# Kernel optimization log

Measured on AMD Instinct MI355X. Metric: run time of the kernel, lower is better.

## Reference

```python
import jax, jax.numpy as jnp
import numpy as np

NEG_INF = -jnp.inf


def setup_inputs() -> dict:
    B, T, E, H = 16, 1024, 1024, 1024  # batch, seq, embed_dim, head_dim (T <= H required by original buffer slicing)
    key = jax.random.key(0)
    k1, k2, k3, k4, k5, k6 = jax.random.split(key, 6)
    return {
        "key": jax.random.normal(k1, (B, T, E), dtype=jnp.float32),
        "query": jax.random.normal(k2, (B, T, E), dtype=jnp.float32),
        "value": jax.random.normal(k3, (B, T, E), dtype=jnp.float32),
        "padding_mask": jnp.zeros((B, 1, T), dtype=jnp.int32),
        # nn.Linear(embed_dim, head_dim, bias=False) weights: [head_dim, embed_dim]
        "Wk": jax.random.normal(k4, (H, E), dtype=jnp.float32) * (E ** -0.5),
        "Wq": jax.random.normal(k5, (H, E), dtype=jnp.float32) * (E ** -0.5),
        "Wv": jax.random.normal(k6, (H, E), dtype=jnp.float32) * (E ** -0.5),
    }


def reference(key, query, value, padding_mask, Wk, Wq, Wv):
    # key/query/value: [B, T, E]; W*: [H, E]
    B, T, E = key.shape
    k = jnp.einsum("bte,he->bth", key, Wk)
    q = jnp.einsum("bte,he->bth", query, Wq)
    v = jnp.einsum("bte,he->bth", value, Wv)
    # NOTE: original scales by d_k = key.size(-1) = embed_dim, not head_dim
    scale = 1.0 / jnp.sqrt(jnp.float32(E))
    qk = jnp.einsum("bth,bsh->bts", q, k) * scale  # [B, T, T]
    # causal buffer is tril(ones, diagonal=1): position i can attend to j <= i+1
    causal = jnp.tril(jnp.ones((T, T), dtype=jnp.float32), k=1)
    qk = jnp.where(causal == 0, NEG_INF, qk)
    qk = jnp.where(padding_mask == 1, NEG_INF, qk)  # padding_mask broadcasts [B,1,T] -> [B,T,T]
    p = jax.nn.softmax(qk, axis=-1)
    attn = jnp.einsum("bts,bsh->bth", p, v)  # dropout is identity in eval mode
    return attn
```

## Files before the change

kernel.cpp:

```cpp
#include <hip/hip_runtime.h>
#include <hip/hip_bf16.h>
#include <stdint.h>

typedef __bf16 bf16;
typedef __attribute__((ext_vector_type(8))) __bf16 bf16x8;
typedef __attribute__((ext_vector_type(4))) __bf16 bf16x4;
typedef __attribute__((ext_vector_type(4))) float  f32x4;

static __device__ __forceinline__ void gll16(const void* g, void* lds_base) {
  __builtin_amdgcn_global_load_lds((__attribute__((address_space(1))) void*)g,
                                   (__attribute__((address_space(3))) void*)lds_base,
                                   16, 0, 0);
}

#define MFMA_CLUSTER(MQ)                                                       \
  __builtin_amdgcn_s_barrier();                                                \
  asm volatile("s_waitcnt lgkmcnt(0)" ::: "memory");                           \
  __builtin_amdgcn_sched_barrier(0);                                           \
  __builtin_amdgcn_s_setprio(1);                                               \
  _Pragma("unroll") for (int i_ = 0; i_ < 4; ++i_)                             \
  _Pragma("unroll") for (int n_ = 0; n_ < 4; ++n_)                             \
  _Pragma("unroll") for (int kh_ = 0; kh_ < 2; ++kh_)                          \
    acc[(MQ) * 4 + i_][n_] = __builtin_amdgcn_mfma_f32_16x16x32_bf16(          \
        af[i_][kh_], bfr[n_][kh_], acc[(MQ) * 4 + i_][n_], 0, 0, 0);           \
  __builtin_amdgcn_s_setprio(0);

template <int VARIANT>
__global__ __launch_bounds__(512, 2) void gemm8(const bf16* __restrict__ A,
                                                const bf16* __restrict__ B,
                                                bf16* __restrict__ Cb,
                                                float* __restrict__ Cf,
                                                const int* __restrict__ pad) {
  extern __shared__ char smem[];
  char* ldsA = smem;
  char* ldsB = smem + 65536;

  const int tid = threadIdx.x;
  const int lane = tid & 63, wave = tid >> 6;
  const int lo = lane & 15, hi = lane >> 4;
  const int wmi = wave >> 2, wni = wave & 3;
  const int swz = (lo & 7) << 4;

  const int nwg = gridDim.x;
  const int id = (blockIdx.x % 8) * (nwg >> 3) + blockIdx.x / 8;

  int row0, col0, nt, b = 0;
  if (VARIANT <= 1) {
    row0 = (id >> 2) * 256; col0 = (id & 3) * 256; nt = 16;
  } else {
    b = id >> 4;
    const int r = id & 15, it = r >> 2, jt = r & 3;
    row0 = it * 256; col0 = jt * 256;
    nt = (VARIANT == 3) ? min(16, 6 + 4 * it) : 16;
    if (VARIANT == 2 && jt > it) {
      bf16* Sb = Cb + ((size_t)b << 20);
      const bf16 NI = (bf16)(-__builtin_inff());
      bf16x8 fill = { NI, NI, NI, NI, NI, NI, NI, NI };
#pragma unroll
      for (int q = 0; q < 16; ++q) {
        const int off = (q * 512 + tid) * 8;
        const int rr = off >> 8, cc = off & 255;
        *(bf16x8*)(Sb + (size_t)(row0 + rr) * 1024 + col0 + cc) = fill;
      }
      return;
    }
  }
  const bf16* Ap = A + ((size_t)b << 20) + (size_t)row0 * 1024;
  const bf16* Bp = B + ((size_t)b << 20) + (size_t)col0 * 1024;
  const int ntm1 = nt - 1;

  auto stgA = [&](int tidx, int slot) {
    const int tc = tidx > ntm1 ? ntm1 : tidx;
#pragma unroll
    for (int r = 0; r < 4; ++r) {
      const int x  = (wave * 4 + r) * 1024 + lane * 16;
      const int xs = x ^ (((x >> 7) & 7) << 4);
      gll16((const char*)Ap + (size_t)(xs >> 7) * 2048 + (size_t)tc * 128 + (xs & 127),
            ldsA + slot * 32768 + (wave * 4 + r) * 1024);
    }
  };
  auto stgB = [&](int tidx, int slot) {
    const int tc = tidx > ntm1 ? ntm1 : tidx;
#pragma unroll
    for (int r = 0; r < 4; ++r) {
      const int x  = (wave * 4 + r) * 1024 + lane * 16;
      const int xs = x ^ (((x >> 7) & 7) << 4);
      gll16((const char*)Bp + (size_t)(xs >> 7) * 2048 + (size_t)tc * 128 + (xs & 127),
            ldsB + slot * 32768 + (wave * 4 + r) * 1024);
    }
  };

  f32x4 acc[8][4] = {};

  stgB(0, 0);
  stgA(0, 0);
  stgB(1, 1);
  asm volatile("s_waitcnt vmcnt(4)" ::: "memory");
  __builtin_amdgcn_s_barrier();

  bf16x8 af[4][2], bfr[4][2];
#pragma unroll 2
  for (int u = 0; u < nt; ++u) {
    const int cur = u & 1;
#pragma unroll
    for (int i_ = 0; i_ < 4; ++i_)
#pragma unroll
      for (int kh_ = 0; kh_ < 2; ++kh_) {
        const int row_ = wmi * 128 + i_ * 16 + lo;
        af[i_][kh_] = *(const bf16x8*)(ldsA + cur * 32768 +
                                       ((row_ * 128 + kh_ * 64 + hi * 16) ^ swz));
      }
#pragma unroll
    for (int n_ = 0; n_ < 4; ++n_)
#pragma unroll
      for (int kh_ = 0; kh_ < 2; ++kh_) {
        const int row_ = wni * 64 + n_ * 16 + lo;
        bfr[n_][kh_] = *(const bf16x8*)(ldsB + cur * 32768 +
                                        ((row_ * 128 + kh_ * 64 + hi * 16) ^ swz));
      }
    stgA(u + 1, cur ^ 1);
    MFMA_CLUSTER(0)
    __builtin_amdgcn_s_barrier();
#pragma unroll
    for (int i_ = 0; i_ < 4; ++i_)
#pragma unroll
      for (int kh_ = 0; kh_ < 2; ++kh_) {
        const int row_ = wmi * 128 + 64 + i_ * 16 + lo;
        af[i_][kh_] = *(const bf16x8*)(ldsA + cur * 32768 +
                                       ((row_ * 128 + kh_ * 64 + hi * 16) ^ swz));
      }
    stgB(u + 2, cur);
    MFMA_CLUSTER(1)
    asm volatile("s_waitcnt vmcnt(4)" ::: "memory");
    __builtin_amdgcn_s_barrier();
  }

  if (VARIANT == 0) {
#pragma unroll
    for (int m = 0; m < 8; ++m)
#pragma unroll
      for (int n = 0; n < 4; ++n) {
        const int c = col0 + wni * 64 + n * 16 + lo;
        const int rbase = row0 + wmi * 128 + m * 16 + hi * 4;
#pragma unroll
        for (int j = 0; j < 4; ++j)
          Cb[(size_t)(rbase + j) * 1024 + c] = (bf16)acc[m][n][j];
      }
  } else if (VARIANT == 1) {
#pragma unroll
    for (int m = 0; m < 8; ++m)
#pragma unroll
      for (int n = 0; n < 4; ++n) {
        const int r = row0 + wmi * 128 + m * 16 + hi * 4;
        const int c = col0 + wni * 64 + n * 16 + lo;
        const int bb = r >> 10, tt = r & 1023;
        bf16x4 h = { (bf16)acc[m][n][0], (bf16)acc[m][n][1],
                     (bf16)acc[m][n][2], (bf16)acc[m][n][3] };
        *(bf16x4*)(Cb + ((size_t)bb << 20) + ((size_t)c << 10) + tt) = h;
      }
  } else if (VARIANT == 2) {
    const float NINF = -__builtin_inff();
#pragma unroll
    for (int n = 0; n < 4; ++n) {
      const int s = col0 + wni * 64 + n * 16 + lo;
      const int pd = pad[(b << 10) + s];
#pragma unroll
      for (int m = 0; m < 8; ++m) {
        const int tbase = row0 + wmi * 128 + m * 16 + hi * 4;
#pragma unroll
        for (int j = 0; j < 4; ++j) {
          float v = acc[m][n][j] * 0.03125f;
          if (s > tbase + j + 1 || pd != 0) v = NINF;
          Cb[((size_t)b << 20) + (size_t)(tbase + j) * 1024 + s] = (bf16)v;
        }
      }
    }
  } else {
#pragma unroll
    for (int m = 0; m < 8; ++m)
#pragma unroll
      for (int n = 0; n < 4; ++n) {
        const int h2 = col0 + wni * 64 + n * 16 + lo;
        const int tbase = row0 + wmi * 128 + m * 16 + hi * 4;
#pragma unroll
        for (int j = 0; j < 4; ++j)
          Cf[((size_t)b << 20) + (size_t)(tbase + j) * 1024 + h2] = acc[m][n][j];
      }
  }
  asm volatile("s_waitcnt vmcnt(0)" ::: "memory");
}

__global__ __launch_bounds__(256) void cvt_kernel(const float* __restrict__ src,
                                                  bf16* __restrict__ dst, int n) {
  const int i = (blockIdx.x * 256 + threadIdx.x) * 8;
  if (i >= n) return;
  const f32x4 a = *(const f32x4*)(src + i);
  const f32x4 b = *(const f32x4*)(src + i + 4);
  bf16x8 o = { (bf16)a[0], (bf16)a[1], (bf16)a[2], (bf16)a[3],
               (bf16)b[0], (bf16)b[1], (bf16)b[2], (bf16)b[3] };
  *(bf16x8*)(dst + i) = o;
}

__global__ __launch_bounds__(64) void corner_kernel(const bf16* __restrict__ Q,
                                                    const bf16* __restrict__ K,
                                                    const int* __restrict__ pad,
                                                    bf16* __restrict__ S) {
  const int b = blockIdx.x / 3, it = blockIdx.x % 3;
  const int t = it * 256 + 255, s = (it + 1) * 256;
  const int lane = threadIdx.x;
  const bf16* q = Q + ((size_t)b << 20) + (size_t)t * 1024 + lane * 16;
  const bf16* k = K + ((size_t)b << 20) + (size_t)s * 1024 + lane * 16;
  bf16x8 q0 = *(const bf16x8*)q, q1 = *(const bf16x8*)(q + 8);
  bf16x8 k0 = *(const bf16x8*)k, k1 = *(const bf16x8*)(k + 8);
  float d = 0.f;
#pragma unroll
  for (int j = 0; j < 8; ++j) d += (float)q0[j] * (float)k0[j] + (float)q1[j] * (float)k1[j];
#pragma unroll
  for (int o = 32; o; o >>= 1) d += __shfl_xor(d, o, 64);
  if (lane == 0) {
    float v = d * 0.03125f;
    if (pad[(b << 10) + s] != 0) v = -__builtin_inff();
    S[((size_t)b << 20) + (size_t)t * 1024 + s] = (bf16)v;
  }
}

__global__ __launch_bounds__(256) void softmax_kernel(bf16* __restrict__ S) {
  const int row  = blockIdx.x * 4 + (threadIdx.x >> 6);
  const int lane = threadIdx.x & 63;
  bf16* r = S + (size_t)row * 1024 + lane * 16;
  bf16x8 v0 = *(const bf16x8*)r;
  bf16x8 v1 = *(const bf16x8*)(r + 8);
  float f[16];
#pragma unroll
  for (int j = 0; j < 8; ++j) { f[j] = (float)v0[j]; f[8 + j] = (float)v1[j]; }
  float m = f[0];
#pragma unroll
  for (int j = 1; j < 16; ++j) m = fmaxf(m, f[j]);
#pragma unroll
  for (int o = 32; o; o >>= 1) m = fmaxf(m, __shfl_xor(m, o, 64));
  float sum = 0.f;
#pragma unroll
  for (int j = 0; j < 16; ++j) { f[j] = __expf(f[j] - m); sum += f[j]; }
#pragma unroll
  for (int o = 32; o; o >>= 1) sum += __shfl_xor(sum, o, 64);
  const float inv = 1.0f / sum;
#pragma unroll
  for (int j = 0; j < 8; ++j) { v0[j] = (bf16)(f[j] * inv); v1[j] = (bf16)(f[8 + j] * inv); }
  *(bf16x8*)r = v0;
  *(bf16x8*)(r + 8) = v1;
}

extern "C" void kernel_launch(void* const* d_in, const int* in_sizes, int n_in,
                              void* d_out, int out_size, void* d_ws, size_t ws_size,
                              hipStream_t stream) {
  const float* key   = (const float*)d_in[0];
  const float* query = (const float*)d_in[1];
  const float* value = (const float*)d_in[2];
  const int*   pad   = (const int*)d_in[3];
  const float* Wk    = (const float*)d_in[4];
  const float* Wq    = (const float*)d_in[5];
  const float* Wv    = (const float*)d_in[6];
  float* out = (float*)d_out;

  bf16* Wkb = (bf16*)d_ws;
  bf16* Wqb = Wkb + (1 << 20);
  bf16* Wvb = Wqb + (1 << 20);
  bf16* qb  = Wvb + (1 << 20);
  bf16* kb  = qb  + (16 << 20);
  bf16* vT  = kb  + (16 << 20);
  bf16* S   = vT  + (16 << 20);
  bf16* Xb  = S;

  hipFuncSetAttribute(reinterpret_cast<const void*>(&gemm8<0>),
                      hipFuncAttributeMaxDynamicSharedMemorySize, 131072);
  hipFuncSetAttribute(reinterpret_cast<const void*>(&gemm8<1>),
                      hipFuncAttributeMaxDynamicSharedMemorySize, 131072);
  hipFuncSetAttribute(reinterpret_cast<const void*>(&gemm8<2>),
                      hipFuncAttributeMaxDynamicSharedMemorySize, 131072);
  hipFuncSetAttribute(reinterpret_cast<const void*>(&gemm8<3>),
                      hipFuncAttributeMaxDynamicSharedMemorySize, 131072);

  cvt_kernel<<<512, 256, 0, stream>>>(Wk, Wkb, 1 << 20);
  cvt_kernel<<<512, 256, 0, stream>>>(Wq, Wqb, 1 << 20);
  cvt_kernel<<<512, 256, 0, stream>>>(Wv, Wvb, 1 << 20);

  cvt_kernel<<<8192, 256, 0, stream>>>(query, Xb, 16 << 20);
  gemm8<0><<<256, 512, 131072, stream>>>(Xb, Wqb, qb, nullptr, nullptr);
  cvt_kernel<<<8192, 256, 0, stream>>>(key, Xb, 16 << 20);
  gemm8<0><<<256, 512, 131072, stream>>>(Xb, Wkb, kb, nullptr, nullptr);
  cvt_kernel<<<8192, 256, 0, stream>>>(value, Xb, 16 << 20);
  gemm8<1><<<256, 512, 131072, stream>>>(Xb, Wvb, vT, nullptr, nullptr);

  gemm8<2><<<256, 512, 131072, stream>>>(qb, kb, S, nullptr, pad);
  corner_kernel<<<48, 64, 0, stream>>>(qb, kb, pad, S);
  softmax_kernel<<<4096, 256, 0, stream>>>(S);
  gemm8<3><<<256, 512, 131072, stream>>>(S, vT, nullptr, out, nullptr);
}
```

Baseline: 261.2 us.

## Skip fully masked score tiles and restrict softmax to causal window

```diff
diff --git a/kernel.cpp b/kernel.cpp
--- a/kernel.cpp
+++ b/kernel.cpp
@@ -51,16 +51,15 @@
     b = id >> 4;
     const int r = id & 15, it = r >> 2, jt = r & 3;
     row0 = it * 256; col0 = jt * 256;
-    nt = (VARIANT == 3) ? min(16, 6 + 4 * it) : 16;
-    if (VARIANT == 2 && jt > it) {
+    nt = (VARIANT == 3) ? min(16, 4 * it + 6) : 16;
+    if (VARIANT == 2 && jt > it + 1) return;
+    if (VARIANT == 2 && jt == it + 1) {
       bf16* Sb = Cb + ((size_t)b << 20);
-      const bf16 NI = (bf16)(-__builtin_inff());
-      bf16x8 fill = { NI, NI, NI, NI, NI, NI, NI, NI };
+      bf16x8 z = {};
 #pragma unroll
       for (int q = 0; q < 16; ++q) {
         const int off = (q * 512 + tid) * 8;
-        const int rr = off >> 8, cc = off & 255;
-        *(bf16x8*)(Sb + (size_t)(row0 + rr) * 1024 + col0 + cc) = fill;
+        *(bf16x8*)(Sb + (size_t)(row0 + (off >> 8)) * 1024 + col0 + (off & 255)) = z;
       }
       return;
     }
@@ -170,7 +169,8 @@
 #pragma unroll
         for (int j = 0; j < 4; ++j) {
           float v = acc[m][n][j] * 0.03125f;
-          if (s > tbase + j + 1 || pd != 0) v = NINF;
+          if (s > tbase + j + 1) v = 0.f;
+          else if (pd != 0) v = NINF;
           Cb[((size_t)b << 20) + (size_t)(tbase + j) * 1024 + s] = (bf16)v;
         }
       }
@@ -194,6 +194,23 @@
                                                   bf16* __restrict__ dst, int n) {
   const int i = (blockIdx.x * 256 + threadIdx.x) * 8;
   if (i >= n) return;
+  const f32x4 a = *(const f32x4*)(src + i);
+  const f32x4 b = *(const f32x4*)(src + i + 4);
+  bf16x8 o = { (bf16)a[0], (bf16)a[1], (bf16)a[2], (bf16)a[3],
+               (bf16)b[0], (bf16)b[1], (bf16)b[2], (bf16)b[3] };
+  *(bf16x8*)(dst + i) = o;
+}
+
+__global__ __launch_bounds__(256) void cvtW_kernel(const float* __restrict__ s0,
+                                                   const float* __restrict__ s1,
+                                                   const float* __restrict__ s2,
+                                                   bf16* __restrict__ d0,
+                                                   bf16* __restrict__ d1,
+                                                   bf16* __restrict__ d2) {
+  const int seg = blockIdx.x >> 9, blk = blockIdx.x & 511;
+  const float* src = seg == 0 ? s0 : (seg == 1 ? s1 : s2);
+  bf16* dst = seg == 0 ? d0 : (seg == 1 ? d1 : d2);
+  const int i = (blk * 256 + threadIdx.x) * 8;
   const f32x4 a = *(const f32x4*)(src + i);
   const f32x4 b = *(const f32x4*)(src + i + 4);
   bf16x8 o = { (bf16)a[0], (bf16)a[1], (bf16)a[2], (bf16)a[3],
@@ -227,27 +244,42 @@
 __global__ __launch_bounds__(256) void softmax_kernel(bf16* __restrict__ S) {
   const int row  = blockIdx.x * 4 + (threadIdx.x >> 6);
   const int lane = threadIdx.x & 63;
+  const int t = row & 1023;
+  const int w = min(1024, t + 2);
+  const bool act = lane * 16 < w;
   bf16* r = S + (size_t)row * 1024 + lane * 16;
-  bf16x8 v0 = *(const bf16x8*)r;
-  bf16x8 v1 = *(const bf16x8*)(r + 8);
+  bf16x8 v0 = {}, v1 = {};
   float f[16];
 #pragma unroll
-  for (int j = 0; j < 8; ++j) { f[j] = (float)v0[j]; f[8 + j] = (float)v1[j]; }
+  for (int j = 0; j < 16; ++j) f[j] = -1e30f;
+  if (act) {
+    v0 = *(const bf16x8*)r;
+    v1 = *(const bf16x8*)(r + 8);
+#pragma unroll
+    for (int j = 0; j < 16; ++j)
+      if (lane * 16 + j < w) f[j] = (float)(j < 8 ? v0[j] : v1[j - 8]);
+  }
   float m = f[0];
 #pragma unroll
   for (int j = 1; j < 16; ++j) m = fmaxf(m, f[j]);
 #pragma unroll
   for (int o = 32; o; o >>= 1) m = fmaxf(m, __shfl_xor(m, o, 64));
   float sum = 0.f;
-#pragma unroll
-  for (int j = 0; j < 16; ++j) { f[j] = __expf(f[j] - m); sum += f[j]; }
+  float e[16];
+#pragma unroll
+  for (int j = 0; j < 16; ++j) { e[j] = __expf(f[j] - m); sum += e[j]; }
 #pragma unroll
   for (int o = 32; o; o >>= 1) sum += __shfl_xor(sum, o, 64);
   const float inv = 1.0f / sum;
-#pragma unroll
-  for (int j = 0; j < 8; ++j) { v0[j] = (bf16)(f[j] * inv); v1[j] = (bf16)(f[8 + j] * inv); }
-  *(bf16x8*)r = v0;
-  *(bf16x8*)(r + 8) = v1;
+  if (act) {
+#pragma unroll
+    for (int j = 0; j < 8; ++j) {
+      v0[j] = (bf16)(lane * 16 + j < w ? e[j] * inv : 0.f);
+      v1[j] = (bf16)(lane * 16 + 8 + j < w ? e[8 + j] * inv : 0.f);
+    }
+    *(bf16x8*)r = v0;
+    *(bf16x8*)(r + 8) = v1;
+  }
 }
 
 extern "C" void kernel_launch(void* const* d_in, const int* in_sizes, int n_in,
@@ -280,9 +312,7 @@
   hipFuncSetAttribute(reinterpret_cast<const void*>(&gemm8<3>),
                       hipFuncAttributeMaxDynamicSharedMemorySize, 131072);
 
-  cvt_kernel<<<512, 256, 0, stream>>>(Wk, Wkb, 1 << 20);
-  cvt_kernel<<<512, 256, 0, stream>>>(Wq, Wqb, 1 << 20);
-  cvt_kernel<<<512, 256, 0, stream>>>(Wv, Wvb, 1 << 20);
+  cvtW_kernel<<<1536, 256, 0, stream>>>(Wk, Wq, Wv, Wkb, Wqb, Wvb);
 
   cvt_kernel<<<8192, 256, 0, stream>>>(query, Xb, 16 << 20);
   gemm8<0><<<256, 512, 131072, stream>>>(Xb, Wqb, qb, nullptr, nullptr);
```

Result: faster. 248.5 us (-4.8%).
